# Kernel tuning notes

Measured on AMD Instinct MI355X. Metric: run time of the kernel, lower is better.

## Reference

```python
import jax, jax.numpy as jnp
import numpy as np

NODES = 23   # 22 players + ball per frame-graph
K = 8        # random neighbors per node
B, T = 64, 128
G = B * T            # total graphs (frames)
N = G * NODES        # total nodes
D_IN, H, RH = 16, 128, 128


def setup_inputs() -> dict:
    key = jax.random.key(0)
    ks = jax.random.split(key, 10)
    x = jax.random.normal(ks[0], (N, D_IN), jnp.float32)
    # per-graph random edges: dst = each node repeated K times, src = random node in same graph
    src_local = jax.random.randint(ks[1], (G, NODES * K), 0, NODES)
    dst_local = jnp.tile(jnp.repeat(jnp.arange(NODES), K)[None, :], (G, 1))
    off = (jnp.arange(G) * NODES)[:, None]
    edge_index = jnp.stack([(src_local + off).reshape(-1),
                            (dst_local + off).reshape(-1)]).astype(jnp.int32)
    runner_idx = jax.random.randint(ks[2], (G,), 0, NODES, dtype=jnp.int32)
    sc = lambda k, sh: (jax.random.normal(k, sh, jnp.float32) * 0.05)
    return {
        'x': x, 'edge_index': edge_index, 'runner_idx': runner_idx,
        'W1': sc(ks[3], (D_IN, H)), 'b1': jnp.zeros((H,), jnp.float32),
        'W2': sc(ks[4], (H, H)),    'b2': jnp.zeros((H,), jnp.float32),
        'W_ih': sc(ks[5], (3 * RH, H)), 'W_hh': sc(ks[6], (3 * RH, RH)),
        'b_ih': jnp.zeros((3 * RH,), jnp.float32), 'b_hh': jnp.zeros((3 * RH,), jnp.float32),
        'Wp': sc(ks[7], (RH, 2)), 'bp': jnp.zeros((2,), jnp.float32),
    }


def _gcn_conv(h, edge_index, W, b):
    # PyG GCNConv: add self-loops, symmetric normalization, scatter-sum
    h = h @ W
    loop = jnp.arange(N, dtype=edge_index.dtype)
    s = jnp.concatenate([edge_index[0], loop])
    d = jnp.concatenate([edge_index[1], loop])
    deg = jax.ops.segment_sum(jnp.ones_like(s, h.dtype), d, num_segments=N)
    dinv = jnp.where(deg > 0, jax.lax.rsqrt(deg), 0.0)
    norm = dinv[s] * dinv[d]                      # [E+N]
    out = jax.ops.segment_sum(h[s] * norm[:, None], d, num_segments=N)
    return out + b


def _gru(seq, W_ih, W_hh, b_ih, b_hh):
    # torch GRU: gates in r,z,n order
    xg = seq @ W_ih.T + b_ih                      # [B,T,3RH]
    def step(hprev, xt):
        gh = hprev @ W_hh.T + b_hh
        xr, xz, xn = jnp.split(xt, 3, axis=-1)
        hr, hz, hn = jnp.split(gh, 3, axis=-1)
        r = jax.nn.sigmoid(xr + hr)
        z = jax.nn.sigmoid(xz + hz)
        n = jnp.tanh(xn + r * hn)
        hnew = (1.0 - z) * n + z * hprev
        return hnew, hnew
    h0 = jnp.zeros((seq.shape[0], RH), seq.dtype)
    _, outs = jax.lax.scan(step, h0, jnp.swapaxes(xg, 0, 1))
    return jnp.swapaxes(outs, 0, 1)               # [B,T,RH]


def reference(x, edge_index, runner_idx, W1, b1, W2, b2,
              W_ih, W_hh, b_ih, b_hh, Wp, bp):
    h = jax.nn.relu(_gcn_conv(x, edge_index, W1, b1))
    h = jax.nn.relu(_gcn_conv(h, edge_index, W2, b2))
    # fused equivalent of the per-graph nonzero()/indexing loop:
    runner_global = jnp.arange(G, dtype=jnp.int32) * NODES + runner_idx
    seq = h[runner_global].reshape(B, T, H)       # all lengths == T, padding is a no-op
    out = _gru(seq, W_ih, W_hh, b_ih, b_hh)
    return out @ Wp + bp                          # [B,T,2]
```

## Files before the change

kernel.cpp:

```cpp
#include <hip/hip_runtime.h>
#include <hip/hip_bf16.h>
#include <math.h>

#define GG 8192
#define NODESN 23
#define KK 8
#define DIN 16
#define HH 128
#define RHH 128
#define EPG (NODESN*KK)
#define TTT 128
#define BBB 64

template<int CTRL>
static __device__ __forceinline__ float dpp_add(float v) {
    int x = __builtin_amdgcn_update_dpp(0, __float_as_int(v), CTRL, 0xF, 0xF, true);
    return v + __int_as_float(x);
}
#define DPP_XOR1 0xB1
#define DPP_XOR2 0x4E
#define DPP_SHL4 0x104

__global__ __launch_bounds__(256) void gcn_hsum(
    const float* __restrict__ x, const int* __restrict__ esrc,
    const int* __restrict__ runner,
    const float* __restrict__ W1, const float* __restrict__ b1,
    float* __restrict__ hsum_g)
{
    __shared__ float xs[NODESN * DIN];
    __shared__ int   srcs[EPG];
    __shared__ float t1[NODESN * HH];
    __shared__ float red[256];

    const int g   = blockIdx.x;
    const int tid = threadIdx.x;
    const int j   = tid & 127;
    const int nh  = tid >> 7;

    for (int i = tid; i < NODESN * DIN; i += 256) xs[i] = x[g * NODESN * DIN + i];
    for (int i = tid; i < EPG; i += 256)          srcs[i] = esrc[g * EPG + i] - g * NODESN;

    float w[DIN];
    #pragma unroll
    for (int k = 0; k < DIN; k++) w[k] = W1[k * HH + j];
    const float b1j = b1[j];
    __syncthreads();

    const int n0 = nh * 12;
    const int n1 = nh ? NODESN : 12;
    for (int n = n0; n < n1; n++) {
        float acc = 0.f;
        #pragma unroll
        for (int k = 0; k < DIN; k += 4) {
            float4 xv = *(const float4*)&xs[n * DIN + k];
            acc = fmaf(xv.x, w[k], fmaf(xv.y, w[k+1], fmaf(xv.z, w[k+2], fmaf(xv.w, w[k+3], acc))));
        }
        t1[n * HH + j] = acc;
    }
    __syncthreads();

    const int r = runner[g];
    float part = 0.f;
    for (int slot = nh; slot < 9; slot += 2) {
        int node = (slot < 8) ? srcs[r * KK + slot] : r;
        float acc = t1[node * HH + j];
        #pragma unroll
        for (int k = 0; k < KK; k++) acc += t1[srcs[node * KK + k] * HH + j];
        part += fmaxf(acc * (1.f / 9.f) + b1j, 0.f);
    }
    red[tid] = part;
    __syncthreads();
    if (tid < HH) hsum_g[(size_t)g * HH + tid] = red[tid] + red[tid + 128];
}

__global__ __launch_bounds__(256) void seq_kernel(
    const float* __restrict__ hsum_g, const float* __restrict__ W2,
    const float* __restrict__ b2, float* __restrict__ seq)
{
    __shared__ float hs[16 * HH];
    const int tid = threadIdx.x;
    const int j = tid & 127, mh = tid >> 7;
    const size_t base = (size_t)blockIdx.x * 16 * HH;

    for (int v = tid; v < 16 * HH / 4; v += 256)
        ((float4*)hs)[v] = ((const float4*)(hsum_g + base))[v];
    __syncthreads();

    float acc[8];
    #pragma unroll
    for (int m = 0; m < 8; m++) acc[m] = 0.f;
    const float* hrow = hs + mh * 8 * HH;
    for (int k = 0; k < HH; k += 4) {
        float w0  = W2[(k+0)*HH + j];
        float w1  = W2[(k+1)*HH + j];
        float w2v = W2[(k+2)*HH + j];
        float w3  = W2[(k+3)*HH + j];
        #pragma unroll
        for (int m = 0; m < 8; m++) {
            float4 hv = *(const float4*)&hrow[m * HH + k];
            acc[m] = fmaf(hv.x, w0, fmaf(hv.y, w1, fmaf(hv.z, w2v, fmaf(hv.w, w3, acc[m]))));
        }
    }
    const float bj = b2[j];
    #pragma unroll
    for (int m = 0; m < 8; m++)
        seq[base + (size_t)(mh * 8 + m) * HH + j] = fmaxf(acc[m] * (1.f/9.f) + bj, 0.f);
}

__global__ void transpose_wih(const float* __restrict__ W, float* __restrict__ WT)
{
    int idx = blockIdx.x * 256 + threadIdx.x;
    if (idx < 3 * RHH * RHH) {
        int jj = idx / RHH, kk = idx - jj * RHH;
        WT[kk * (3 * RHH) + jj] = W[idx];
    }
}

__global__ __launch_bounds__(384) void xg_kernel(
    const float* __restrict__ seq, const float* __restrict__ WT,
    const float* __restrict__ b_ih, float* __restrict__ xg)
{
    const int tid = threadIdx.x;
    const int m0 = blockIdx.x * 8;
    const float* srow = seq + (size_t)m0 * RHH;
    float acc[8];
    const float bv = b_ih[tid];
    #pragma unroll
    for (int mi = 0; mi < 8; mi++) acc[mi] = bv;
    for (int k = 0; k < RHH; k += 4) {
        float w0 = WT[(k+0)*384 + tid];
        float w1 = WT[(k+1)*384 + tid];
        float w2 = WT[(k+2)*384 + tid];
        float w3 = WT[(k+3)*384 + tid];
        #pragma unroll
        for (int mi = 0; mi < 8; mi++) {
            float4 sv = *(const float4*)(srow + mi * RHH + k);
            acc[mi] = fmaf(sv.x, w0, fmaf(sv.y, w1, fmaf(sv.z, w2, fmaf(sv.w, w3, acc[mi]))));
        }
    }
    #pragma unroll
    for (int mi = 0; mi < 8; mi++)
        xg[(size_t)(m0 + mi) * 384 + tid] = acc[mi];
}

#define CHUNK 32
#define XGB_FLOATS (CHUNK * HH * 4)

__global__ __launch_bounds__(512)
__attribute__((amdgpu_waves_per_eu(2, 2)))
void gru_kernel(
    const float* __restrict__ xg, const float* __restrict__ W_hh,
    const float* __restrict__ b_hh, const float* __restrict__ Wp,
    const float* __restrict__ bp, float* __restrict__ out)
{
    __shared__ float xgbuf[XGB_FLOATS];
    __shared__ float houtb[(CHUNK + 2) * HH];
    __shared__ float wps[2 * RHH + 2];

    const int b   = blockIdx.x;
    const int tid = threadIdx.x;
    const int q   = tid & 3;
    const int i   = tid >> 2;

    float4 wrv[8], wzv[8], wnv[8];
    int lof[8];
    {
        const float* br = W_hh + (size_t)i * RHH + q * 32;
        const float* bz = br + (size_t)RHH * RHH;
        const float* bn = bz + (size_t)RHH * RHH;
        #pragma unroll
        for (int m = 0; m < 8; m++) {
            int p = (m + 2 * q) & 7;
            lof[m] = q * 32 + 4 * p;
            wrv[m] = *(const float4*)(br + 4 * p);
            wzv[m] = *(const float4*)(bz + 4 * p);
            wnv[m] = *(const float4*)(bn + 4 * p);
        }
    }
    const float bhr = b_hh[i];
    const float bhz = b_hh[RHH + i];
    const float bhn = b_hh[2 * RHH + i];

    if (tid < 2 * RHH) wps[tid] = Wp[tid];
    if (tid < 2)       wps[2 * RHH + tid] = bp[tid];
    if (tid < HH)      houtb[CHUNK * HH + tid] = 0.f;
    float hprev = 0.f;

    const float* xbase = xg + (size_t)b * TTT * 3 * RHH;
    float* outb = out + (size_t)b * TTT * 2;

    for (int c = 0; c < TTT / CHUNK; c++) {
        #pragma unroll
        for (int k2 = 0; k2 < 8; k2++) {
            int slot = tid + (k2 << 9);
            int tl = slot >> 7, ii = slot & 127;
            const float* gsrc = xbase + (size_t)(c * CHUNK + tl) * 384 + ii;
            float4 v;
            v.x = gsrc[0]; v.y = gsrc[128]; v.z = gsrc[256]; v.w = 0.f;
            *(float4*)&xgbuf[slot << 2] = v;
        }
        if (c > 0) {
            const int s  = tid & 7;
            const int cc = (tid >> 3) & 1;
            const int tl = tid >> 4;
            const float* hr = &houtb[(tl + 1) * HH + s * 16];
            float acc = 0.f;
            #pragma unroll
            for (int m = 0; m < 16; m += 4) {
                float4 hv = *(const float4*)(hr + m);
                int k = s * 16 + m;
                acc = fmaf(hv.x, wps[(k+0)*2 + cc],
                      fmaf(hv.y, wps[(k+1)*2 + cc],
                      fmaf(hv.z, wps[(k+2)*2 + cc],
                      fmaf(hv.w, wps[(k+3)*2 + cc], acc))));
            }
            acc = dpp_add<DPP_XOR1>(acc);
            acc = dpp_add<DPP_XOR2>(acc);
            acc = dpp_add<DPP_SHL4>(acc);
            if (s == 0)
                outb[((c - 1) * CHUNK + tl) * 2 + cc] = acc + wps[2 * RHH + cc];
        }
        __syncthreads();

        for (int tl = 0; tl < CHUNK; tl++) {
            const float* hrow = &houtb[(tl == 0 ? CHUNK : tl) * HH];
            float4 xgv = *(const float4*)&xgbuf[(tl * HH + i) << 2];
            float ar = 0.f, az = 0.f, an = 0.f;
            #pragma unroll
            for (int m = 0; m < 8; m++) {
                float4 hv = *(const float4*)(hrow + lof[m]);
                ar = fmaf(hv.x, wrv[m].x, fmaf(hv.y, wrv[m].y, fmaf(hv.z, wrv[m].z, fmaf(hv.w, wrv[m].w, ar))));
                az = fmaf(hv.x, wzv[m].x, fmaf(hv.y, wzv[m].y, fmaf(hv.z, wzv[m].z, fmaf(hv.w, wzv[m].w, az))));
                an = fmaf(hv.x, wnv[m].x, fmaf(hv.y, wnv[m].y, fmaf(hv.z, wnv[m].z, fmaf(hv.w, wnv[m].w, an))));
            }
            ar = dpp_add<DPP_XOR1>(ar); ar = dpp_add<DPP_XOR2>(ar);
            az = dpp_add<DPP_XOR1>(az); az = dpp_add<DPP_XOR2>(az);
            an = dpp_add<DPP_XOR1>(an); an = dpp_add<DPP_XOR2>(an);

            float sr = xgv.x + ar + bhr;
            float sz = xgv.y + az + bhz;
            float rg = 1.f / (1.f + __expf(-sr));
            float zg = 1.f / (1.f + __expf(-sz));
            float tv = fmaf(rg, an + bhn, xgv.z);
            tv = fminf(fmaxf(tv, -15.f), 15.f);
            float e2 = __expf(-2.f * tv);
            float ng = (1.f - e2) / (1.f + e2);
            hprev = fmaf(zg, hprev, (1.f - zg) * ng);
            if (q == 0) houtb[(tl + 1) * HH + i] = hprev;
            __syncthreads();
        }
    }

    {
        const int s  = tid & 7;
        const int cc = (tid >> 3) & 1;
        const int tl = tid >> 4;
        const float* hr = &houtb[(tl + 1) * HH + s * 16];
        float acc = 0.f;
        #pragma unroll
        for (int m = 0; m < 16; m += 4) {
            float4 hv = *(const float4*)(hr + m);
            int k = s * 16 + m;
            acc = fmaf(hv.x, wps[(k+0)*2 + cc],
                  fmaf(hv.y, wps[(k+1)*2 + cc],
                  fmaf(hv.z, wps[(k+2)*2 + cc],
                  fmaf(hv.w, wps[(k+3)*2 + cc], acc))));
        }
        acc = dpp_add<DPP_XOR1>(acc);
        acc = dpp_add<DPP_XOR2>(acc);
        acc = dpp_add<DPP_SHL4>(acc);
        if (s == 0)
            outb[((TTT / CHUNK - 1) * CHUNK + tl) * 2 + cc] = acc + wps[2 * RHH + cc];
    }
}

extern "C" void kernel_launch(void* const* d_in, const int* in_sizes, int n_in,
                              void* d_out, int out_size, void* d_ws, size_t ws_size,
                              hipStream_t stream)
{
    const float* x      = (const float*)d_in[0];
    const int*   eidx   = (const int*)d_in[1];
    const int*   runner = (const int*)d_in[2];
    const float* W1     = (const float*)d_in[3];
    const float* b1     = (const float*)d_in[4];
    const float* W2     = (const float*)d_in[5];
    const float* b2     = (const float*)d_in[6];
    const float* W_ih   = (const float*)d_in[7];
    const float* W_hh   = (const float*)d_in[8];
    const float* b_ih   = (const float*)d_in[9];
    const float* b_hh   = (const float*)d_in[10];
    const float* Wp     = (const float*)d_in[11];
    const float* bp     = (const float*)d_in[12];
    float* out = (float*)d_out;

    float* seq    = (float*)d_ws;
    float* xg     = seq + (size_t)GG * HH;
    float* WT     = xg + (size_t)GG * 3 * RHH;
    float* hsum_g = xg;

    transpose_wih<<<192, 256, 0, stream>>>(W_ih, WT);
    gcn_hsum<<<GG, 256, 0, stream>>>(x, eidx, runner, W1, b1, hsum_g);
    seq_kernel<<<GG / 16, 256, 0, stream>>>(hsum_g, W2, b2, seq);
    xg_kernel<<<GG / 8, 384, 0, stream>>>(seq, WT, b_ih, xg);
    gru_kernel<<<BBB, 512, 0, stream>>>(xg, W_hh, b_hh, Wp, bp, out);
}
```

Measured before the change: 241.8 us.

## Split GRU matvec over 8 lanes computing two hidden units each

```diff
diff --git a/kernel.cpp b/kernel.cpp
--- a/kernel.cpp
+++ b/kernel.cpp
@@ -19,6 +19,7 @@
 }
 #define DPP_XOR1 0xB1
 #define DPP_XOR2 0x4E
+#define DPP_MIR7 0x141
 #define DPP_SHL4 0x104
 
 __global__ __launch_bounds__(256) void gcn_hsum(
@@ -159,27 +160,30 @@
 
     const int b   = blockIdx.x;
     const int tid = threadIdx.x;
-    const int q   = tid & 3;
-    const int i   = tid >> 2;
-
-    float4 wrv[8], wzv[8], wnv[8];
-    int lof[8];
+    const int kq  = tid & 7;
+    const int i0  = tid >> 3;
+    const int uhf = kq >> 2;
+    const int u   = 2 * i0 + uhf;
+
+    float4 wr0[4], wz0[4], wn0[4], wr1[4], wz1[4], wn1[4];
+    int hof[4];
     {
-        const float* br = W_hh + (size_t)i * RHH + q * 32;
-        const float* bz = br + (size_t)RHH * RHH;
-        const float* bn = bz + (size_t)RHH * RHH;
-        #pragma unroll
-        for (int m = 0; m < 8; m++) {
-            int p = (m + 2 * q) & 7;
-            lof[m] = q * 32 + 4 * p;
-            wrv[m] = *(const float4*)(br + 4 * p);
-            wzv[m] = *(const float4*)(bz + 4 * p);
-            wnv[m] = *(const float4*)(bn + 4 * p);
-        }
-    }
-    const float bhr = b_hh[i];
-    const float bhz = b_hh[RHH + i];
-    const float bhn = b_hh[2 * RHH + i];
+        const float* w0 = W_hh + (size_t)(2 * i0) * RHH + kq * 16;
+        #pragma unroll
+        for (int m = 0; m < 4; m++) {
+            const int off = 4 * ((m + kq) & 3);
+            hof[m] = kq * 16 + off;
+            wr0[m] = *(const float4*)(w0 + off);
+            wz0[m] = *(const float4*)(w0 + RHH * RHH + off);
+            wn0[m] = *(const float4*)(w0 + 2 * RHH * RHH + off);
+            wr1[m] = *(const float4*)(w0 + RHH + off);
+            wz1[m] = *(const float4*)(w0 + RHH * RHH + RHH + off);
+            wn1[m] = *(const float4*)(w0 + 2 * RHH * RHH + RHH + off);
+        }
+    }
+    const float bhr = b_hh[u];
+    const float bhz = b_hh[RHH + u];
+    const float bhn = b_hh[2 * RHH + u];
 
     if (tid < 2 * RHH) wps[tid] = Wp[tid];
     if (tid < 2)       wps[2 * RHH + tid] = bp[tid];
@@ -222,20 +226,35 @@
         }
         __syncthreads();
 
+        float4 xgv = *(const float4*)&xgbuf[u << 2];
         for (int tl = 0; tl < CHUNK; tl++) {
             const float* hrow = &houtb[(tl == 0 ? CHUNK : tl) * HH];
-            float4 xgv = *(const float4*)&xgbuf[(tl * HH + i) << 2];
-            float ar = 0.f, az = 0.f, an = 0.f;
+            float4 xgn = xgv;
+            if (tl + 1 < CHUNK)
+                xgn = *(const float4*)&xgbuf[((tl + 1) * HH + u) << 2];
+
+            float ar0 = 0.f, az0 = 0.f, an0 = 0.f;
+            float ar1 = 0.f, az1 = 0.f, an1 = 0.f;
             #pragma unroll
-            for (int m = 0; m < 8; m++) {
-                float4 hv = *(const float4*)(hrow + lof[m]);
-                ar = fmaf(hv.x, wrv[m].x, fmaf(hv.y, wrv[m].y, fmaf(hv.z, wrv[m].z, fmaf(hv.w, wrv[m].w, ar))));
-                az = fmaf(hv.x, wzv[m].x, fmaf(hv.y, wzv[m].y, fmaf(hv.z, wzv[m].z, fmaf(hv.w, wzv[m].w, az))));
-                an = fmaf(hv.x, wnv[m].x, fmaf(hv.y, wnv[m].y, fmaf(hv.z, wnv[m].z, fmaf(hv.w, wnv[m].w, an))));
+            for (int m = 0; m < 4; m++) {
+                float4 hv = *(const float4*)(hrow + hof[m]);
+                ar0 = fmaf(hv.x, wr0[m].x, fmaf(hv.y, wr0[m].y, fmaf(hv.z, wr0[m].z, fmaf(hv.w, wr0[m].w, ar0))));
+                az0 = fmaf(hv.x, wz0[m].x, fmaf(hv.y, wz0[m].y, fmaf(hv.z, wz0[m].z, fmaf(hv.w, wz0[m].w, az0))));
+                an0 = fmaf(hv.x, wn0[m].x, fmaf(hv.y, wn0[m].y, fmaf(hv.z, wn0[m].z, fmaf(hv.w, wn0[m].w, an0))));
+                ar1 = fmaf(hv.x, wr1[m].x, fmaf(hv.y, wr1[m].y, fmaf(hv.z, wr1[m].z, fmaf(hv.w, wr1[m].w, ar1))));
+                az1 = fmaf(hv.x, wz1[m].x, fmaf(hv.y, wz1[m].y, fmaf(hv.z, wz1[m].z, fmaf(hv.w, wz1[m].w, az1))));
+                an1 = fmaf(hv.x, wn1[m].x, fmaf(hv.y, wn1[m].y, fmaf(hv.z, wn1[m].z, fmaf(hv.w, wn1[m].w, an1))));
             }
-            ar = dpp_add<DPP_XOR1>(ar); ar = dpp_add<DPP_XOR2>(ar);
-            az = dpp_add<DPP_XOR1>(az); az = dpp_add<DPP_XOR2>(az);
-            an = dpp_add<DPP_XOR1>(an); an = dpp_add<DPP_XOR2>(an);
+            ar0 = dpp_add<DPP_XOR1>(ar0); ar0 = dpp_add<DPP_XOR2>(ar0); ar0 = dpp_add<DPP_MIR7>(ar0);
+            az0 = dpp_add<DPP_XOR1>(az0); az0 = dpp_add<DPP_XOR2>(az0); az0 = dpp_add<DPP_MIR7>(az0);
+            an0 = dpp_add<DPP_XOR1>(an0); an0 = dpp_add<DPP_XOR2>(an0); an0 = dpp_add<DPP_MIR7>(an0);
+            ar1 = dpp_add<DPP_XOR1>(ar1); ar1 = dpp_add<DPP_XOR2>(ar1); ar1 = dpp_add<DPP_MIR7>(ar1);
+            az1 = dpp_add<DPP_XOR1>(az1); az1 = dpp_add<DPP_XOR2>(az1); az1 = dpp_add<DPP_MIR7>(az1);
+            an1 = dpp_add<DPP_XOR1>(an1); an1 = dpp_add<DPP_XOR2>(an1); an1 = dpp_add<DPP_MIR7>(an1);
+
+            float ar = uhf ? ar1 : ar0;
+            float az = uhf ? az1 : az0;
+            float an = uhf ? an1 : an0;
 
             float sr = xgv.x + ar + bhr;
             float sz = xgv.y + az + bhz;
@@ -246,7 +265,8 @@
             float e2 = __expf(-2.f * tv);
             float ng = (1.f - e2) / (1.f + e2);
             hprev = fmaf(zg, hprev, (1.f - zg) * ng);
-            if (q == 0) houtb[(tl + 1) * HH + i] = hprev;
+            if ((kq & 3) == 0) houtb[(tl + 1) * HH + u] = hprev;
+            xgv = xgn;
             __syncthreads();
         }
     }
```

After: 245.7 us. About the same (+1.6%).

## Split GRU hidden-unit dot products across 8 lanes with 1024-thread blocks

Applied to the files above, without the earlier changes.

```diff
diff --git a/kernel.cpp b/kernel.cpp
--- a/kernel.cpp
+++ b/kernel.cpp
@@ -19,6 +19,7 @@
 }
 #define DPP_XOR1 0xB1
 #define DPP_XOR2 0x4E
+#define DPP_MIR7 0x141
 #define DPP_SHL4 0x104
 
 __global__ __launch_bounds__(256) void gcn_hsum(
@@ -146,8 +147,8 @@
 #define CHUNK 32
 #define XGB_FLOATS (CHUNK * HH * 4)
 
-__global__ __launch_bounds__(512)
-__attribute__((amdgpu_waves_per_eu(2, 2)))
+__global__ __launch_bounds__(1024)
+__attribute__((amdgpu_waves_per_eu(4, 4)))
 void gru_kernel(
     const float* __restrict__ xg, const float* __restrict__ W_hh,
     const float* __restrict__ b_hh, const float* __restrict__ Wp,
@@ -159,22 +160,20 @@
 
     const int b   = blockIdx.x;
     const int tid = threadIdx.x;
-    const int q   = tid & 3;
-    const int i   = tid >> 2;
-
-    float4 wrv[8], wzv[8], wnv[8];
-    int lof[8];
+    const int kq  = tid & 7;
+    const int i   = tid >> 3;
+
+    float4 wr[4], wz[4], wn[4];
+    int hof[4];
     {
-        const float* br = W_hh + (size_t)i * RHH + q * 32;
-        const float* bz = br + (size_t)RHH * RHH;
-        const float* bn = bz + (size_t)RHH * RHH;
-        #pragma unroll
-        for (int m = 0; m < 8; m++) {
-            int p = (m + 2 * q) & 7;
-            lof[m] = q * 32 + 4 * p;
-            wrv[m] = *(const float4*)(br + 4 * p);
-            wzv[m] = *(const float4*)(bz + 4 * p);
-            wnv[m] = *(const float4*)(bn + 4 * p);
+        const float* w0 = W_hh + (size_t)i * RHH + kq * 16;
+        #pragma unroll
+        for (int m = 0; m < 4; m++) {
+            const int off = 4 * ((m + kq) & 3);
+            hof[m] = kq * 16 + off;
+            wr[m] = *(const float4*)(w0 + off);
+            wz[m] = *(const float4*)(w0 + RHH * RHH + off);
+            wn[m] = *(const float4*)(w0 + 2 * RHH * RHH + off);
         }
     }
     const float bhr = b_hh[i];
@@ -191,15 +190,15 @@
 
     for (int c = 0; c < TTT / CHUNK; c++) {
         #pragma unroll
-        for (int k2 = 0; k2 < 8; k2++) {
-            int slot = tid + (k2 << 9);
+        for (int k2 = 0; k2 < 4; k2++) {
+            int slot = tid + (k2 << 10);
             int tl = slot >> 7, ii = slot & 127;
             const float* gsrc = xbase + (size_t)(c * CHUNK + tl) * 384 + ii;
             float4 v;
             v.x = gsrc[0]; v.y = gsrc[128]; v.z = gsrc[256]; v.w = 0.f;
             *(float4*)&xgbuf[slot << 2] = v;
         }
-        if (c > 0) {
+        if (c > 0 && tid < 512) {
             const int s  = tid & 7;
             const int cc = (tid >> 3) & 1;
             const int tl = tid >> 4;
@@ -222,20 +221,24 @@
         }
         __syncthreads();
 
+        float4 xgv = *(const float4*)&xgbuf[i << 2];
         for (int tl = 0; tl < CHUNK; tl++) {
             const float* hrow = &houtb[(tl == 0 ? CHUNK : tl) * HH];
-            float4 xgv = *(const float4*)&xgbuf[(tl * HH + i) << 2];
+            float4 xgn = xgv;
+            if (tl + 1 < CHUNK)
+                xgn = *(const float4*)&xgbuf[((tl + 1) * HH + i) << 2];
+
             float ar = 0.f, az = 0.f, an = 0.f;
             #pragma unroll
-            for (int m = 0; m < 8; m++) {
-                float4 hv = *(const float4*)(hrow + lof[m]);
-                ar = fmaf(hv.x, wrv[m].x, fmaf(hv.y, wrv[m].y, fmaf(hv.z, wrv[m].z, fmaf(hv.w, wrv[m].w, ar))));
-                az = fmaf(hv.x, wzv[m].x, fmaf(hv.y, wzv[m].y, fmaf(hv.z, wzv[m].z, fmaf(hv.w, wzv[m].w, az))));
-                an = fmaf(hv.x, wnv[m].x, fmaf(hv.y, wnv[m].y, fmaf(hv.z, wnv[m].z, fmaf(hv.w, wnv[m].w, an))));
+            for (int m = 0; m < 4; m++) {
+                float4 hv = *(const float4*)(hrow + hof[m]);
+                ar = fmaf(hv.x, wr[m].x, fmaf(hv.y, wr[m].y, fmaf(hv.z, wr[m].z, fmaf(hv.w, wr[m].w, ar))));
+                az = fmaf(hv.x, wz[m].x, fmaf(hv.y, wz[m].y, fmaf(hv.z, wz[m].z, fmaf(hv.w, wz[m].w, az))));
+                an = fmaf(hv.x, wn[m].x, fmaf(hv.y, wn[m].y, fmaf(hv.z, wn[m].z, fmaf(hv.w, wn[m].w, an))));
             }
-            ar = dpp_add<DPP_XOR1>(ar); ar = dpp_add<DPP_XOR2>(ar);
-            az = dpp_add<DPP_XOR1>(az); az = dpp_add<DPP_XOR2>(az);
-            an = dpp_add<DPP_XOR1>(an); an = dpp_add<DPP_XOR2>(an);
+            ar = dpp_add<DPP_XOR1>(ar); ar = dpp_add<DPP_XOR2>(ar); ar = dpp_add<DPP_MIR7>(ar);
+            az = dpp_add<DPP_XOR1>(az); az = dpp_add<DPP_XOR2>(az); az = dpp_add<DPP_MIR7>(az);
+            an = dpp_add<DPP_XOR1>(an); an = dpp_add<DPP_XOR2>(an); an = dpp_add<DPP_MIR7>(an);
 
             float sr = xgv.x + ar + bhr;
             float sz = xgv.y + az + bhz;
@@ -246,12 +249,13 @@
             float e2 = __expf(-2.f * tv);
             float ng = (1.f - e2) / (1.f + e2);
             hprev = fmaf(zg, hprev, (1.f - zg) * ng);
-            if (q == 0) houtb[(tl + 1) * HH + i] = hprev;
+            if (kq == 0) houtb[(tl + 1) * HH + i] = hprev;
+            xgv = xgn;
             __syncthreads();
         }
     }
 
-    {
+    if (tid < 512) {
         const int s  = tid & 7;
         const int cc = (tid >> 3) & 1;
         const int tl = tid >> 4;
@@ -302,5 +306,5 @@
     gcn_hsum<<<GG, 256, 0, stream>>>(x, eidx, runner, W1, b1, hsum_g);
     seq_kernel<<<GG / 16, 256, 0, stream>>>(hsum_g, W2, b2, seq);
     xg_kernel<<<GG / 8, 384, 0, stream>>>(seq, WT, b_ih, xg);
-    gru_kernel<<<BBB, 512, 0, stream>>>(xg, W_hh, b_hh, Wp, bp, out);
-}
+    gru_kernel<<<BBB, 1024, 0, stream>>>(xg, W_hh, b_hh, Wp, bp, out);
+}
```

Measured after the change: 266.9 us. 1.1x slower.
